# Kernel optimization log

Hardware: AMD Instinct MI355X
Metric: run time of the kernel (lower is better)

The kernel has to match this reference:

```python
import jax, jax.numpy as jnp
import numpy as np

HIDDEN = 512


def setup_inputs() -> dict:
    key = jax.random.key(0)
    ks = jax.random.split(key, 5)
    S, B, I, H = 256, 128, 1024, HIDDEN
    scale_ih = 1.0 / np.sqrt(H)
    return {
        "x": jax.random.normal(ks[0], (S, B, I), dtype=jnp.float32),
        "w_ih": jax.random.normal(ks[1], (4 * H, I), dtype=jnp.float32) * scale_ih,
        "w_hh": jax.random.normal(ks[2], (4 * H, H), dtype=jnp.float32) * scale_ih,
        "b_ih": jax.random.normal(ks[3], (4 * H,), dtype=jnp.float32) * scale_ih,
        "b_hh": jax.random.normal(ks[4], (4 * H,), dtype=jnp.float32) * scale_ih,
    }


def reference(x, w_ih, w_hh, b_ih, b_hh):
    # x: [S, B, I]. LSTMCell with PyTorch gate order (i, f, g, o).
    S, B, _ = x.shape
    H = HIDDEN
    bias = b_ih + b_hh  # fuse both biases

    def step(carry, xt):
        h, c = carry
        gates = xt @ w_ih.T + h @ w_hh.T + bias  # [B, 4H]
        i, f, g, o = jnp.split(gates, 4, axis=-1)
        i = jax.nn.sigmoid(i)
        f = jax.nn.sigmoid(f)
        g = jnp.tanh(g)
        o = jax.nn.sigmoid(o)
        c = f * c + i * g
        h = o * jnp.tanh(c)
        # original code's h[arange(B)] / c[arange(B)] is an identity gather: no-op
        return (h, c), None

    h0 = jnp.zeros((B, H), dtype=x.dtype)
    c0 = jnp.zeros((B, H), dtype=x.dtype)
    (h, c), _ = jax.lax.scan(step, (h0, c0), x)
    return h.sum()
```

## Files before the change

kernel.cpp:

```cpp
#include <hip/hip_runtime.h>

typedef __attribute__((ext_vector_type(8))) short short8;
typedef __attribute__((ext_vector_type(4))) float f32x4;
typedef __attribute__((ext_vector_type(4))) int i32x4;

#define S_LEN 256
#define BATCH 128
#define IN_DIM 1024
#define HID 512
#define G4 2048

#define SENT 0xFFFFFFFFu

#define LSTM_BLOCKS 128
#define GEMM_WORKERS 128
#define TOT_BLOCKS (LSTM_BLOCKS + GEMM_WORKERS)
#define NT_PER_ROW 8
#define N_TILES (256 * NT_PER_ROW)

__device__ unsigned g_cnt[S_LEN];

__device__ __forceinline__ unsigned short f32_bf16(float f) {
  unsigned int u = __float_as_uint(f);
  u = (u + 0x7FFFu + ((u >> 16) & 1u)) >> 16;
  return (unsigned short)u;
}
__device__ __forceinline__ float bf16_f32(unsigned short h) {
  return __uint_as_float(((unsigned int)h) << 16);
}
__device__ __forceinline__ float sigm(float x) { return 1.0f / (1.0f + __expf(-x)); }
__device__ __forceinline__ float tanh_fast(float x) {
  return 1.0f - 2.0f / (__expf(2.0f * x) + 1.0f);
}
__device__ __forceinline__ unsigned ld_cnt(const unsigned* p) {
  return __hip_atomic_load(p, __ATOMIC_RELAXED, __HIP_MEMORY_SCOPE_AGENT);
}
__device__ __forceinline__ unsigned ld_u32_agent(const void* p) {
  return __hip_atomic_load((const unsigned*)p, __ATOMIC_RELAXED, __HIP_MEMORY_SCOPE_AGENT);
}
__device__ __forceinline__ short8 pin8(short8 x) {
  i32x4 t = __builtin_bit_cast(i32x4, x);
  asm volatile("" : "+v"(t));
  return __builtin_bit_cast(short8, t);
}

__device__ __forceinline__ void cvt4(const float* __restrict__ s,
                                     unsigned short* __restrict__ d, int i) {
  float4 v = *(const float4*)(s + (size_t)i * 4);
  ushort4 o;
  o.x = f32_bf16(v.x); o.y = f32_bf16(v.y); o.z = f32_bf16(v.z); o.w = f32_bf16(v.w);
  *(ushort4*)(d + (size_t)i * 4) = o;
}

__global__ void prep(const float* __restrict__ w_ih, const float* __restrict__ w_hh,
                     const float* __restrict__ b_ih, const float* __restrict__ b_hh,
                     unsigned short* __restrict__ wih_bf, unsigned short* __restrict__ whh_bf,
                     float* __restrict__ bias, uint4* __restrict__ hring4) {
  const int gtid = blockIdx.x * blockDim.x + threadIdx.x;
  const int gsz = gridDim.x * blockDim.x;
  if (gtid < G4) bias[gtid] = b_ih[gtid] + b_hh[gtid];
  if (gtid < S_LEN) g_cnt[gtid] = 0u;
  for (int i = gtid; i < 2097152 / 4; i += gsz) cvt4(w_ih, wih_bf, i);
  for (int i = gtid; i < 1048576 / 4; i += gsz) cvt4(w_hh, whh_bf, i);
  const int SLOT4 = BATCH * HID / 8;
  const int TOT4 = 257 * SLOT4;
  const uint4 z = make_uint4(0u, 0u, 0u, 0u);
  const uint4 sN = make_uint4(SENT, SENT, SENT, SENT);
  for (int k = gtid; k < TOT4; k += gsz) hring4[k] = (k < SLOT4) ? z : sN;
}

__device__ __forceinline__ void gl_lds16(const void* g, void* l) {
  __builtin_amdgcn_global_load_lds(
      (const __attribute__((address_space(1))) unsigned int*)g,
      (__attribute__((address_space(3))) unsigned int*)l, 16, 0, 0);
}

__global__ __launch_bounds__(512, 1) void fused_lstm(
    const unsigned short* __restrict__ whh,
    const float* __restrict__ x,
    const unsigned short* __restrict__ wih,
    const float* __restrict__ bias,
    unsigned short* __restrict__ gx,
    unsigned* __restrict__ hring,
    float* __restrict__ out) {
  __shared__ __align__(16) union {
    struct { unsigned short Hs[2][16][520]; float Gt[16][132]; } L;
    struct { unsigned short As[2 * 4096]; unsigned short Bs[2 * 8192]; } G;
  } sm;

  const int tid = threadIdx.x;
  const int w = tid >> 6, l = tid & 63;

  if (blockIdx.x >= LSTM_BLOCKS) {
    const int wm = w & 1, wn = w >> 1;
    const int arow = tid >> 2, akc = tid & 3;
    for (int tile = (int)blockIdx.x - LSTM_BLOCKS; tile < N_TILES; tile += GEMM_WORKERS) {
      const int nt = tile & (NT_PER_ROW - 1), mt = tile >> 3;
      f32x4 acc[4][4];
#pragma unroll
      for (int i = 0; i < 4; i++)
#pragma unroll
        for (int j = 0; j < 4; j++) acc[i][j] = f32x4{0.f, 0.f, 0.f, 0.f};

      const float* xrow = x + (size_t)(mt * 128 + arow) * 1024 + akc * 8;

      auto issueB = [&](int cur, int k0) {
#pragma unroll
        for (int jj = 0; jj < 2; ++jj) {
          int cid = jj * 512 + tid;
          int row = cid >> 2, kc = cid & 3;
          gl_lds16(wih + (size_t)(nt * 256 + row) * 1024 + k0 + kc * 8,
                   sm.G.Bs + cur * 8192 + jj * 4096 + w * 512);
        }
      };
      auto issueX = [&](int k0, float4& xa, float4& xb) {
        xa = *(const float4*)(xrow + k0);
        xb = *(const float4*)(xrow + k0 + 4);
      };
      auto commitX = [&](int cur, const float4& xa, const float4& xb) {
        uint4 o;
        o.x = (unsigned)f32_bf16(xa.x) | ((unsigned)f32_bf16(xa.y) << 16);
        o.y = (unsigned)f32_bf16(xa.z) | ((unsigned)f32_bf16(xa.w) << 16);
        o.z = (unsigned)f32_bf16(xb.x) | ((unsigned)f32_bf16(xb.y) << 16);
        o.w = (unsigned)f32_bf16(xb.z) | ((unsigned)f32_bf16(xb.w) << 16);
        *(uint4*)&sm.G.As[cur * 4096 + tid * 8] = o;
      };

      float4 xa, xb;
      issueX(0, xa, xb);
      issueB(0, 0);
      commitX(0, xa, xb);
      asm volatile("s_waitcnt vmcnt(0) lgkmcnt(0)" ::: "memory");
      __builtin_amdgcn_s_barrier();

      for (int ks = 0; ks < 32; ++ks) {
        const int cur = ks & 1;
        if (ks + 1 < 32) {
          issueX((ks + 1) * 32, xa, xb);
          issueB(cur ^ 1, (ks + 1) * 32);
        }
        short8 a[4], b[4];
#pragma unroll
        for (int i = 0; i < 4; i++)
          a[i] = *(const short8*)&sm.G.As[cur * 4096 +
                                          (wm * 64 + i * 16 + (l & 15)) * 32 + (l >> 4) * 8];
#pragma unroll
        for (int j = 0; j < 4; j++)
          b[j] = *(const short8*)&sm.G.Bs[cur * 8192 +
                                          (wn * 64 + j * 16 + (l & 15)) * 32 + (l >> 4) * 8];
#pragma unroll
        for (int i = 0; i < 4; i++)
#pragma unroll
          for (int j = 0; j < 4; j++)
            acc[i][j] = __builtin_amdgcn_mfma_f32_16x16x32_bf16(a[i], b[j], acc[i][j], 0, 0, 0);
        if (ks + 1 < 32) commitX(cur ^ 1, xa, xb);
        __builtin_amdgcn_sched_barrier(0);
        asm volatile("s_waitcnt vmcnt(0) lgkmcnt(0)" ::: "memory");
        __builtin_amdgcn_s_barrier();
      }

#pragma unroll
      for (int j = 0; j < 4; j++) {
        int cg = nt * 256 + wn * 64 + j * 16 + (l & 15);
        float bv = bias[cg];
#pragma unroll
        for (int i = 0; i < 4; i++) {
          int rbase = mt * 128 + wm * 64 + i * 16 + (l >> 4) * 4;
#pragma unroll
          for (int r = 0; r < 4; r++) {
            unsigned short hv = f32_bf16(acc[i][j][r] + bv);
            __hip_atomic_store(gx + (size_t)(rbase + r) * G4 + cg, hv,
                               __ATOMIC_RELAXED, __HIP_MEMORY_SCOPE_AGENT);
          }
        }
      }
      asm volatile("s_waitcnt vmcnt(0)" ::: "memory");
      __syncthreads();
      if (tid == 0)
        __hip_atomic_fetch_add(&g_cnt[mt], 1u, __ATOMIC_RELAXED, __HIP_MEMORY_SCOPE_AGENT);
    }
    return;
  }

  __builtin_amdgcn_s_setprio(1);
  if (tid >= 256) {
    for (int t = 0; t < S_LEN; t++) __syncthreads();
    return;
  }
  const int m = blockIdx.x & 7;
  const int s = blockIdx.x >> 3;

  short8 bw[16][2];
#pragma unroll
  for (int u = 0; u < 2; u++) {
    int n = (2 * w + u) * 16 + (l & 15);
    int jn = n >> 2, g = n & 3;
    int R = g * 512 + s * 32 + jn;
    const unsigned short* base = whh + (size_t)R * 512 + ((l >> 4) * 8);
#pragma unroll
    for (int kk = 0; kk < 16; kk++) bw[kk][u] = pin8(*(const short8*)(base + kk * 32));
  }

  const int b = l & 15;
  const int p = 4 * w + (l >> 4);
  const int gb = m * 16 + b;
  const int colg = s * 32 + 2 * p;
  float c0 = 0.f, c1 = 0.f;
  unsigned hp_last = 0u;

  const int SLOTW = BATCH * HID / 2;
  const unsigned long long* hull = (const unsigned long long*)hring;
  const int SLOTQ = BATCH * HID / 4;

  const int skc = tid & 127;
  const int srow = tid >> 7;
  const bool selfst = (((tid >> 3) & 15) == s);
  const size_t qbase = (size_t)(m * 16 + srow) * 128 + skc;

  unsigned long long v[8];
#pragma unroll
  for (int it = 0; it < 8; it++)
    v[it] = __hip_atomic_load(&hull[qbase + (size_t)it * 256],
                              __ATOMIC_RELAXED, __HIP_MEMORY_SCOPE_AGENT);
  while (ld_cnt(&g_cnt[0]) != (unsigned)NT_PER_ROW) __builtin_amdgcn_s_sleep(2);
  float2 pg[4];
  {
    size_t base0 = (size_t)gb * G4 + colg;
#pragma unroll
    for (int g = 0; g < 4; g++) {
      unsigned u = ld_u32_agent(gx + base0 + (size_t)g * 512);
      pg[g].x = bf16_f32((unsigned short)(u & 0xFFFFu));
      pg[g].y = bf16_f32((unsigned short)(u >> 16));
    }
  }
  unsigned cn = ld_cnt(&g_cnt[1]);

  for (int t = 0; t < S_LEN; t++) {
    const int buf = t & 1;
    const unsigned long long* src = hull + (size_t)t * SLOTQ;

    if (!(selfst && t > 0)) {
      for (;;) {
        int bad = 0;
#pragma unroll
        for (int it = 0; it < 8; it++)
          bad |= (((unsigned)v[it] == SENT) | ((unsigned)(v[it] >> 32) == SENT)) << it;
        if (!bad) break;
#pragma unroll
        for (int it = 0; it < 8; it++)
          if ((bad >> it) & 1)
            v[it] = __hip_atomic_load(&src[qbase + (size_t)it * 256],
                                      __ATOMIC_RELAXED, __HIP_MEMORY_SCOPE_AGENT);
      }
#pragma unroll
      for (int it = 0; it < 8; it++)
        *(unsigned long long*)&sm.L.Hs[buf][it * 2 + srow][skc * 4] = v[it];
    }
    __syncthreads();

    unsigned long long vn[8];
    float2 pgn[4];
    if (t + 1 < S_LEN) {
      if (!selfst) {
        const unsigned long long* srcn = hull + (size_t)(t + 1) * SLOTQ;
#pragma unroll
        for (int it = 0; it < 8; it++)
          vn[it] = __hip_atomic_load(&srcn[qbase + (size_t)it * 256],
                                     __ATOMIC_RELAXED, __HIP_MEMORY_SCOPE_AGENT);
      }
      if (cn != (unsigned)NT_PER_ROW) {
        do {
          __builtin_amdgcn_s_sleep(1);
          cn = ld_cnt(&g_cnt[t + 1]);
        } while (cn != (unsigned)NT_PER_ROW);
      }
      size_t basen = (size_t)((t + 1) * BATCH + gb) * G4 + colg;
#pragma unroll
      for (int g = 0; g < 4; g++) {
        unsigned u = ld_u32_agent(gx + basen + (size_t)g * 512);
        pgn[g].x = bf16_f32((unsigned short)(u & 0xFFFFu));
        pgn[g].y = bf16_f32((unsigned short)(u >> 16));
      }
      cn = (t + 2 < S_LEN) ? ld_cnt(&g_cnt[t + 2]) : (unsigned)NT_PER_ROW;
    }

    f32x4 acc0 = f32x4{0.f, 0.f, 0.f, 0.f};
    f32x4 acc1 = f32x4{0.f, 0.f, 0.f, 0.f};
#pragma unroll
    for (int kk = 0; kk < 16; kk++) {
      short8 a = *(const short8*)&sm.L.Hs[buf][l & 15][kk * 32 + (l >> 4) * 8];
      acc0 = __builtin_amdgcn_mfma_f32_16x16x32_bf16(a, bw[kk][0], acc0, 0, 0, 0);
      acc1 = __builtin_amdgcn_mfma_f32_16x16x32_bf16(a, bw[kk][1], acc1, 0, 0, 0);
    }

#pragma unroll
    for (int r = 0; r < 4; r++) {
      sm.L.Gt[(l >> 4) * 4 + r][(2 * w + 0) * 16 + (l & 15)] = acc0[r];
      sm.L.Gt[(l >> 4) * 4 + r][(2 * w + 1) * 16 + (l & 15)] = acc1[r];
    }

    float4 g0 = *(const float4*)&sm.L.Gt[b][8 * p];
    float4 g1 = *(const float4*)&sm.L.Gt[b][8 * p + 4];
    float i0 = sigm(g0.x + pg[0].x), f0 = sigm(g0.y + pg[1].x);
    float gg0 = tanh_fast(g0.z + pg[2].x), o0 = sigm(g0.w + pg[3].x);
    c0 = f0 * c0 + i0 * gg0;
    float h0 = o0 * tanh_fast(c0);
    float i1 = sigm(g1.x + pg[0].y), f1 = sigm(g1.y + pg[1].y);
    float gg1 = tanh_fast(g1.z + pg[2].y), o1 = sigm(g1.w + pg[3].y);
    c1 = f1 * c1 + i1 * gg1;
    float h1 = o1 * tanh_fast(c1);
    unsigned hp = (unsigned)f32_bf16(h0) | ((unsigned)f32_bf16(h1) << 16);
    hp_last = hp;

    __hip_atomic_store(&hring[(size_t)(t + 1) * SLOTW + gb * 256 + s * 16 + p], hp,
                       __ATOMIC_RELAXED, __HIP_MEMORY_SCOPE_AGENT);
    *(unsigned*)&sm.L.Hs[buf ^ 1][b][colg] = hp;

#pragma unroll
    for (int it = 0; it < 8; it++) v[it] = vn[it];
#pragma unroll
    for (int g = 0; g < 4; g++) pg[g] = pgn[g];
  }

  {
    float loc = bf16_f32((unsigned short)(hp_last & 0xFFFFu)) +
                bf16_f32((unsigned short)(hp_last >> 16));
#pragma unroll
    for (int off = 32; off > 0; off >>= 1) loc += __shfl_down(loc, off);
    if (l == 0) atomicAdd(out, loc);
  }
}

extern "C" void kernel_launch(void* const* d_in, const int* in_sizes, int n_in,
                              void* d_out, int out_size, void* d_ws, size_t ws_size,
                              hipStream_t stream) {
  const float* x = (const float*)d_in[0];
  const float* w_ih = (const float*)d_in[1];
  const float* w_hh = (const float*)d_in[2];
  const float* b_ih = (const float*)d_in[3];
  const float* b_hh = (const float*)d_in[4];

  char* ws = (char*)d_ws;
  unsigned short* wih_bf = (unsigned short*)(ws + 67108864);
  unsigned short* whh_bf = (unsigned short*)(ws + 71303168);
  float* bias = (float*)(ws + 73400320);
  unsigned* hring = (unsigned*)(ws + 73408512);
  unsigned short* gx = (unsigned short*)(ws + 107094016);

  prep<<<1024, 256, 0, stream>>>(w_ih, w_hh, b_ih, b_hh, wih_bf, whh_bf, bias,
                                 (uint4*)hring);

  fused_lstm<<<TOT_BLOCKS, 512, 0, stream>>>(whh_bf, x, wih_bf, bias, gx, hring,
                                             (float*)d_out);
}
```

Baseline: 1.107 ms.

## Remap GEMM worker tiles by XCD and drop register pinning of W_hh

GEMM worker blocks now get a fixed N-tile and walk M-tiles with stride 8, grouped so each worker's x row-blocks stay on the same XCD (wid&7). The W_ih slice a block uses then stays resident in that XCD's L2, and x reuse across the eight N-tiles is localized. This also changes the order in which M-tiles finish, which affects when the recurrent LSTM blocks can start consuming gx. Separately, the inline-asm pin on the W_hh register loads is removed, leaving the compiler free to schedule or rematerialize them, with a risk of reloads or spills.

```diff
diff --git a/kernel.cpp b/kernel.cpp
--- a/kernel.cpp
+++ b/kernel.cpp
@@ -2,7 +2,6 @@
 
 typedef __attribute__((ext_vector_type(8))) short short8;
 typedef __attribute__((ext_vector_type(4))) float f32x4;
-typedef __attribute__((ext_vector_type(4))) int i32x4;
 
 #define S_LEN 256
 #define BATCH 128
@@ -37,11 +36,6 @@
 }
 __device__ __forceinline__ unsigned ld_u32_agent(const void* p) {
   return __hip_atomic_load((const unsigned*)p, __ATOMIC_RELAXED, __HIP_MEMORY_SCOPE_AGENT);
-}
-__device__ __forceinline__ short8 pin8(short8 x) {
-  i32x4 t = __builtin_bit_cast(i32x4, x);
-  asm volatile("" : "+v"(t));
-  return __builtin_bit_cast(short8, t);
 }
 
 __device__ __forceinline__ void cvt4(const float* __restrict__ s,
@@ -92,15 +86,21 @@
   const int w = tid >> 6, l = tid & 63;
 
   if (blockIdx.x >= LSTM_BLOCKS) {
+    const int wid = (int)blockIdx.x - LSTM_BLOCKS;
+    const int xcd = wid & 7;
+    const int kk8 = wid >> 3;
+    const int pp = kk8 >> 3;
+    const int nt = kk8 & 7;
     const int wm = w & 1, wn = w >> 1;
     const int arow = tid >> 2, akc = tid & 3;
-    for (int tile = (int)blockIdx.x - LSTM_BLOCKS; tile < N_TILES; tile += GEMM_WORKERS) {
-      const int nt = tile & (NT_PER_ROW - 1), mt = tile >> 3;
+
+    for (int j = 0; j < 16; ++j) {
+      const int mt = xcd + 8 * (2 * j + pp);
       f32x4 acc[4][4];
 #pragma unroll
       for (int i = 0; i < 4; i++)
 #pragma unroll
-        for (int j = 0; j < 4; j++) acc[i][j] = f32x4{0.f, 0.f, 0.f, 0.f};
+        for (int jj = 0; jj < 4; jj++) acc[i][jj] = f32x4{0.f, 0.f, 0.f, 0.f};
 
       const float* xrow = x + (size_t)(mt * 128 + arow) * 1024 + akc * 8;
 
@@ -145,14 +145,15 @@
           a[i] = *(const short8*)&sm.G.As[cur * 4096 +
                                           (wm * 64 + i * 16 + (l & 15)) * 32 + (l >> 4) * 8];
 #pragma unroll
-        for (int j = 0; j < 4; j++)
-          b[j] = *(const short8*)&sm.G.Bs[cur * 8192 +
-                                          (wn * 64 + j * 16 + (l & 15)) * 32 + (l >> 4) * 8];
+        for (int jj = 0; jj < 4; jj++)
+          b[jj] = *(const short8*)&sm.G.Bs[cur * 8192 +
+                                           (wn * 64 + jj * 16 + (l & 15)) * 32 + (l >> 4) * 8];
 #pragma unroll
         for (int i = 0; i < 4; i++)
 #pragma unroll
-          for (int j = 0; j < 4; j++)
-            acc[i][j] = __builtin_amdgcn_mfma_f32_16x16x32_bf16(a[i], b[j], acc[i][j], 0, 0, 0);
+          for (int jj = 0; jj < 4; jj++)
+            acc[i][jj] =
+                __builtin_amdgcn_mfma_f32_16x16x32_bf16(a[i], b[jj], acc[i][jj], 0, 0, 0);
         if (ks + 1 < 32) commitX(cur ^ 1, xa, xb);
         __builtin_amdgcn_sched_barrier(0);
         asm volatile("s_waitcnt vmcnt(0) lgkmcnt(0)" ::: "memory");
@@ -160,15 +161,15 @@
       }
 
 #pragma unroll
-      for (int j = 0; j < 4; j++) {
-        int cg = nt * 256 + wn * 64 + j * 16 + (l & 15);
+      for (int jj = 0; jj < 4; jj++) {
+        int cg = nt * 256 + wn * 64 + jj * 16 + (l & 15);
         float bv = bias[cg];
 #pragma unroll
         for (int i = 0; i < 4; i++) {
           int rbase = mt * 128 + wm * 64 + i * 16 + (l >> 4) * 4;
 #pragma unroll
           for (int r = 0; r < 4; r++) {
-            unsigned short hv = f32_bf16(acc[i][j][r] + bv);
+            unsigned short hv = f32_bf16(acc[i][jj][r] + bv);
             __hip_atomic_store(gx + (size_t)(rbase + r) * G4 + cg, hv,
                                __ATOMIC_RELAXED, __HIP_MEMORY_SCOPE_AGENT);
           }
@@ -198,7 +199,7 @@
     int R = g * 512 + s * 32 + jn;
     const unsigned short* base = whh + (size_t)R * 512 + ((l >> 4) * 8);
 #pragma unroll
-    for (int kk = 0; kk < 16; kk++) bw[kk][u] = pin8(*(const short8*)(base + kk * 32));
+    for (int kk = 0; kk < 16; kk++) bw[kk][u] = *(const short8*)(base + kk * 32);
   }
 
   const int b = l & 15;
```

Result: faster. 1.057 ms (-4.5%).
